# Optimization experiments

Measured on AMD Instinct MI355X. Metric: run time of the kernel, lower is better.

Reference implementation:

```python
import jax, jax.numpy as jnp
import numpy as np

B, S, HID = 2, 2048, 2048
NH, NKV, D = 16, 4, 128
EPS = 1e-6
THETA = 1000000.0
SCALE = D ** -0.5


def _rmsnorm(x, w):
    # per-head RMSNorm over last dim (head_dim)
    var = jnp.mean(x * x, axis=-1, keepdims=True)
    return x * jax.lax.rsqrt(var + EPS) * w


def _rope(pos, x):
    # neox-style rotary over full head_dim. x: [B,S,h,D], pos: [B,S]
    half = D // 2
    inv_freq = THETA ** (-jnp.arange(half, dtype=jnp.float32) / half)  # theta^(-2i/D)
    freqs = pos.astype(jnp.float32)[..., None] * inv_freq              # [B,S,half]
    cos = jnp.cos(freqs)[:, :, None, :]
    sin = jnp.sin(freqs)[:, :, None, :]
    x1, x2 = x[..., :half], x[..., half:]
    return jnp.concatenate([x1 * cos - x2 * sin, x2 * cos + x1 * sin], axis=-1)


def setup_inputs() -> dict:
    key = jax.random.key(0)
    ks = jax.random.split(key, 6)
    hidden_states = jax.random.normal(ks[0], (B, S, HID), dtype=jnp.float32)
    positions = jnp.tile(jnp.arange(S, dtype=jnp.int32)[None, :], (B, 1))
    sd = 0.02
    Wq = jax.random.normal(ks[1], (HID, NH * D), dtype=jnp.float32) * sd
    Wk = jax.random.normal(ks[2], (HID, NKV * D), dtype=jnp.float32) * sd
    Wv = jax.random.normal(ks[3], (HID, NKV * D), dtype=jnp.float32) * sd
    Wo = jax.random.normal(ks[4], (NH * D, HID), dtype=jnp.float32) * sd
    q_norm_w = jnp.ones((D,), dtype=jnp.float32)
    k_norm_w = jnp.ones((D,), dtype=jnp.float32)
    return {"hidden_states": hidden_states, "positions": positions,
            "Wq": Wq, "Wk": Wk, "Wv": Wv, "Wo": Wo,
            "q_norm_w": q_norm_w, "k_norm_w": k_norm_w}


def reference(hidden_states, positions, Wq, Wk, Wv, Wo, q_norm_w, k_norm_w):
    # QKV projections (no bias)
    q = (hidden_states @ Wq).reshape(B, S, NH, D)
    k = (hidden_states @ Wk).reshape(B, S, NKV, D)
    v = (hidden_states @ Wv).reshape(B, S, NKV, D)
    # per-head RMSNorm
    q = _rmsnorm(q, q_norm_w)
    k = _rmsnorm(k, k_norm_w)
    # rotary embedding
    q = _rope(positions, q)
    k = _rope(positions, k)
    # GQA: expand kv heads to q heads
    rep = NH // NKV
    k = jnp.repeat(k, rep, axis=2)  # [B,S,NH,D]
    v = jnp.repeat(v, rep, axis=2)
    # non-causal (ENCODER_ONLY) attention
    scores = jnp.einsum('bqhd,bkhd->bhqk', q, k) * SCALE
    attn = jax.nn.softmax(scores, axis=-1)
    ctx = jnp.einsum('bhqk,bkhd->bqhd', attn, v).reshape(B, S, NH * D)
    out = ctx @ Wo
    return out
```

## Files before the change

kernel.cpp:

```cpp
#include <hip/hip_runtime.h>

typedef unsigned short ushort_t;
typedef __attribute__((ext_vector_type(8))) short short8;
typedef __attribute__((ext_vector_type(4))) float f32x4;

#define Bb 2
#define Ss 2048
#define HID 2048
#define NH 16
#define NKV 4
#define Dd 128
constexpr float EPS_ = 1e-6f;
constexpr float THETA_ = 1000000.0f;
constexpr float SCALE_ = 0.08838834764831845f;
constexpr float C2_ = 0.12753785f;

__device__ __forceinline__ ushort_t f2bf(float x) {
  union { float f; unsigned u; } v; v.f = x;
  unsigned r = (v.u + 0x7fffu + ((v.u >> 16) & 1u)) >> 16;
  return (ushort_t)r;
}
__device__ __forceinline__ float bf2f(ushort_t u) {
  union { unsigned u; float f; } v; v.u = ((unsigned)u) << 16;
  return v.f;
}

typedef const __attribute__((address_space(1))) void* gas1_t;
typedef __attribute__((address_space(3))) void* las3_t;
__device__ __forceinline__ void gload_lds16(const void* g, void* l) {
  __builtin_amdgcn_global_load_lds((gas1_t)g, (las3_t)l, 16, 0, 0);
}

__device__ __forceinline__ void store_out(float* p, float v) { *p = v; }
__device__ __forceinline__ void store_out(ushort_t* p, float v) { *p = f2bf(v); }

__global__ __launch_bounds__(256) void convert_f32_bf16(
    const float* __restrict__ src, ushort_t* __restrict__ dst, long n) {
  long i = ((long)blockIdx.x * 256 + threadIdx.x) * 4;
  if (i + 3 < n) {
    float4 v = *(const float4*)(src + i);
    ushort_t o0 = f2bf(v.x), o1 = f2bf(v.y), o2 = f2bf(v.z), o3 = f2bf(v.w);
    ushort_t* d = dst + i;
    d[0] = o0; d[1] = o1; d[2] = o2; d[3] = o3;
  }
}

__global__ __launch_bounds__(256) void transpose_f32_bf16(
    const float* __restrict__ src, ushort_t* __restrict__ dst, int R, int C) {
  __shared__ float tile[32][33];
  int c0 = blockIdx.x * 32, r0 = blockIdx.y * 32;
  int tx = threadIdx.x & 31, ty = threadIdx.x >> 5;
#pragma unroll
  for (int j = 0; j < 4; j++)
    tile[ty + j * 8][tx] = src[(long)(r0 + ty + j * 8) * C + c0 + tx];
  __syncthreads();
#pragma unroll
  for (int j = 0; j < 4; j++)
    dst[(long)(c0 + ty + j * 8) * R + r0 + tx] = f2bf(tile[tx][ty + j * 8]);
}

template <typename OutT>
__global__ __launch_bounds__(256) void gemm_bt(
    const ushort_t* __restrict__ A, const ushort_t* __restrict__ Bt,
    OutT* __restrict__ C, int M, int N, int K) {
  __shared__ __align__(16) ushort_t As[128 * 32];
  __shared__ __align__(16) ushort_t Bs[128 * 32];
  const int t = threadIdx.x;
  const int wave = t >> 6, lane = t & 63;
  const int wr = wave >> 1, wc = wave & 1;
  const int quad = lane >> 4, l16 = lane & 15;
  const long bm = (long)blockIdx.y * 128, bn = (long)blockIdx.x * 128;

  f32x4 acc[4][4] = {};

  const int srow = t >> 2, schunk = t & 3;
  const ushort_t* aSrc = A + (bm + srow) * (long)K + schunk * 8;
  const ushort_t* bSrc = Bt + (bn + srow) * (long)K + schunk * 8;
  const int ldsOff = srow * 32 + schunk * 8;

  for (int k0 = 0; k0 < K; k0 += 32) {
    __syncthreads();
    gload_lds16(aSrc + k0, &As[ldsOff]);
    gload_lds16(aSrc + (long)64 * K + k0, &As[ldsOff + 64 * 32]);
    gload_lds16(bSrc + k0, &Bs[ldsOff]);
    gload_lds16(bSrc + (long)64 * K + k0, &Bs[ldsOff + 64 * 32]);
    __syncthreads();
    short8 af[4], bf[4];
#pragma unroll
    for (int i = 0; i < 4; i++) {
      af[i] = *(const short8*)&As[(wr * 64 + i * 16 + l16) * 32 + quad * 8];
      bf[i] = *(const short8*)&Bs[(wc * 64 + i * 16 + l16) * 32 + quad * 8];
    }
#pragma unroll
    for (int i = 0; i < 4; i++)
#pragma unroll
      for (int j = 0; j < 4; j++)
        acc[i][j] = __builtin_amdgcn_mfma_f32_16x16x32_bf16(af[i], bf[j], acc[i][j], 0, 0, 0);
  }
#pragma unroll
  for (int i = 0; i < 4; i++)
#pragma unroll
    for (int j = 0; j < 4; j++)
#pragma unroll
      for (int r = 0; r < 4; r++) {
        long rr = bm + wr * 64 + i * 16 + quad * 4 + r;
        long cc = bn + wc * 64 + j * 16 + l16;
        store_out(&C[rr * N + cc], acc[i][j][r]);
      }
}

__global__ __launch_bounds__(256) void rmsnorm_rope(
    ushort_t* __restrict__ qkv, const int* __restrict__ positions,
    const float* __restrict__ qw, const float* __restrict__ kw) {
  int gw = blockIdx.x * 4 + (threadIdx.x >> 6);
  int lane = threadIdx.x & 63;
  int bs = gw / 20, h = gw % 20;
  ushort_t* src = qkv + (long)bs * 3072 + h * 128;
  float x0 = bf2f(src[lane]), x1 = bf2f(src[lane + 64]);
  float ss = x0 * x0 + x1 * x1;
#pragma unroll
  for (int off = 32; off; off >>= 1) ss += __shfl_xor(ss, off);
  float r = rsqrtf(ss * (1.0f / 128.0f) + EPS_);
  const float* w = (h < 16) ? qw : kw;
  x0 = x0 * r * w[lane];
  x1 = x1 * r * w[lane + 64];
  float pos = (float)positions[bs];
  float inv_freq = powf(THETA_, -(float)lane * (1.0f / 64.0f));
  float f = pos * inv_freq;
  float sn, cs;
  sincosf(f, &sn, &cs);
  float o0 = x0 * cs - x1 * sn;
  float o1 = x1 * cs + x0 * sn;
  src[lane] = f2bf(o0);
  src[lane + 64] = f2bf(o1);
}

__global__ __launch_bounds__(256) void transpose_v(
    const ushort_t* __restrict__ qkv, ushort_t* __restrict__ Vt) {
  __shared__ ushort_t tile[64][65];
  int bh = blockIdx.z;
  int s0 = blockIdx.x * 64, d0 = blockIdx.y * 64;
  int b = bh >> 2, hk = bh & 3;
  int tx = threadIdx.x & 63, ty = threadIdx.x >> 6;
#pragma unroll
  for (int j = 0; j < 16; j++) {
    int sl = j * 4 + ty;
    tile[sl][tx] = qkv[(long)(b * Ss + s0 + sl) * 3072 + 2560 + hk * 128 + d0 + tx];
  }
  __syncthreads();
  const long vtbase = (long)bh * Dd * Ss;
#pragma unroll
  for (int j = 0; j < 16; j++) {
    int dl = j * 4 + ty;
    Vt[vtbase + (long)(d0 + dl) * Ss + s0 + tx] = tile[tx][dl];
  }
}

__global__ __launch_bounds__(512) void flash_attn(
    const ushort_t* __restrict__ qkv, const ushort_t* __restrict__ Vt,
    ushort_t* __restrict__ ctx) {
  __shared__ __align__(16) ushort_t Ks[2][64 * 128];
  __shared__ __align__(16) ushort_t Vs[2][128 * 64];
  __shared__ __align__(16) ushort_t Ps[8][16 * 64];
  const int qt = blockIdx.x, h = blockIdx.y, b = blockIdx.z;
  const int hk = h >> 2;
  const int t = threadIdx.x, wave = t >> 6, lane = t & 63;
  const int quad = lane >> 4, l16 = lane & 15;

  const ushort_t* qp = qkv + (long)(b * Ss + qt * 128) * 3072 + h * 128;
  const ushort_t* kp = qkv + (long)(b * Ss) * 3072 + 2048 + hk * 128;
  const ushort_t* vp = Vt + ((long)(b * NKV + hk) * Dd) * Ss;

  auto stage = [&](int kt, int bi) {
    const int k0 = kt * 64;
#pragma unroll
    for (int it = 0; it < 2; it++) {
      int tt = t + it * 512;
      int row = tt >> 4, cl = tt & 15, cg = cl ^ (row & 15);
      gload_lds16(kp + (long)(k0 + row) * 3072 + cg * 8, &Ks[bi][tt * 8]);
    }
#pragma unroll
    for (int it = 0; it < 2; it++) {
      int tt = t + it * 512;
      int row = tt >> 3, cl = tt & 7, cg = cl ^ (row & 7);
      gload_lds16(vp + (long)row * Ss + k0 + cg * 8, &Vs[bi][tt * 8]);
    }
  };

  stage(0, 0);

  short8 qf[4];
  {
    const ushort_t* qrow = qp + (long)(wave * 16 + l16) * 3072 + quad * 8;
#pragma unroll
    for (int kc = 0; kc < 4; kc++)
      qf[kc] = *(const short8*)(qrow + kc * 32);
  }

  float m_i[4] = {-1e30f, -1e30f, -1e30f, -1e30f};
  float l_i[4] = {0.f, 0.f, 0.f, 0.f};
  f32x4 o[8] = {};

  asm volatile("s_waitcnt vmcnt(0)" ::: "memory");
  __syncthreads();

  int cur = 0;
  for (int kt = 0; kt < Ss / 64; kt++) {
    if (kt + 1 < Ss / 64) stage(kt + 1, cur ^ 1);

    f32x4 sa[4] = {};
#pragma unroll
    for (int kc = 0; kc < 4; kc++) {
#pragma unroll
      for (int nt = 0; nt < 4; nt++) {
        int brow = nt * 16 + l16;
        short8 bfr = *(const short8*)&Ks[cur][brow * 128 + (((kc * 4 + quad) ^ (brow & 15)) * 8)];
        sa[nt] = __builtin_amdgcn_mfma_f32_16x16x32_bf16(qf[kc], bfr, sa[nt], 0, 0, 0);
      }
    }

    float mc[4], alpha[4];
#pragma unroll
    for (int r = 0; r < 4; r++) {
      float mx = fmaxf(fmaxf(sa[0][r], sa[1][r]), fmaxf(sa[2][r], sa[3][r]));
#pragma unroll
      for (int off = 8; off; off >>= 1) mx = fmaxf(mx, __shfl_xor(mx, off));
      float mnew = fmaxf(m_i[r], mx);
      alpha[r] = __builtin_amdgcn_exp2f((m_i[r] - mnew) * C2_);
      m_i[r] = mnew;
      mc[r] = mnew * C2_;
    }
    float rs[4] = {0.f, 0.f, 0.f, 0.f};
#pragma unroll
    for (int nt = 0; nt < 4; nt++)
#pragma unroll
      for (int r = 0; r < 4; r++) {
        float p = __builtin_amdgcn_exp2f(__builtin_fmaf(sa[nt][r], C2_, -mc[r]));
        sa[nt][r] = p;
        rs[r] += p;
      }
#pragma unroll
    for (int r = 0; r < 4; r++) {
#pragma unroll
      for (int off = 8; off; off >>= 1) rs[r] += __shfl_xor(rs[r], off);
      l_i[r] = l_i[r] * alpha[r] + rs[r];
    }
#pragma unroll
    for (int nt = 0; nt < 4; nt++)
#pragma unroll
      for (int r = 0; r < 4; r++) {
        int row = quad * 4 + r, col = nt * 16 + l16;
        int cg = col >> 3, ci = col & 7;
        int cl = cg ^ (row & 7);
        union { float f; unsigned u; } pv; pv.f = sa[nt][r];
        Ps[wave][row * 64 + cl * 8 + ci] = (ushort_t)((pv.u + 0x8000u) >> 16);
      }
#pragma unroll
    for (int dt = 0; dt < 8; dt++)
#pragma unroll
      for (int r = 0; r < 4; r++) o[dt][r] *= alpha[r];
    asm volatile("s_waitcnt lgkmcnt(0)" ::: "memory");
#pragma unroll
    for (int kc = 0; kc < 2; kc++) {
      int arow = l16;
      short8 af = *(const short8*)&Ps[wave][arow * 64 + (((kc * 4 + quad) ^ (arow & 7)) * 8)];
#pragma unroll
      for (int dt = 0; dt < 8; dt++) {
        int brow = dt * 16 + l16;
        short8 bfr = *(const short8*)&Vs[cur][brow * 64 + (((kc * 4 + quad) ^ (brow & 7)) * 8)];
        o[dt] = __builtin_amdgcn_mfma_f32_16x16x32_bf16(af, bfr, o[dt], 0, 0, 0);
      }
    }

    asm volatile("s_waitcnt vmcnt(0)" ::: "memory");
    __syncthreads();
    cur ^= 1;
  }
  const long obase = (long)(b * Ss + qt * 128 + wave * 16) * (NH * Dd) + h * Dd;
#pragma unroll
  for (int dt = 0; dt < 8; dt++)
#pragma unroll
    for (int r = 0; r < 4; r++) {
      int row = quad * 4 + r, col = dt * 16 + l16;
      ctx[obase + (long)row * (NH * Dd) + col] = f2bf(o[dt][r] / l_i[r]);
    }
}

extern "C" void kernel_launch(void* const* d_in, const int* in_sizes, int n_in,
                              void* d_out, int out_size, void* d_ws, size_t ws_size,
                              hipStream_t stream) {
  const float* hidden = (const float*)d_in[0];
  const int* positions = (const int*)d_in[1];
  const float* Wq = (const float*)d_in[2];
  const float* Wk = (const float*)d_in[3];
  const float* Wv = (const float*)d_in[4];
  const float* Wo = (const float*)d_in[5];
  const float* qw = (const float*)d_in[6];
  const float* kw = (const float*)d_in[7];
  float* out = (float*)d_out;

  char* ws = (char*)d_ws;
  ushort_t* Xbf = (ushort_t*)(ws);
  ushort_t* WqkvT = (ushort_t*)(ws + (16l << 20));
  ushort_t* WoT = (ushort_t*)(ws + (28l << 20));
  ushort_t* qkvb = (ushort_t*)(ws + (36l << 20));
  ushort_t* Vt = (ushort_t*)(ws + (60l << 20));
  ushort_t* ctx = Xbf;

  const long nX = (long)Bb * Ss * HID;
  convert_f32_bf16<<<(unsigned)(nX / 4 / 256), 256, 0, stream>>>(hidden, Xbf, nX);
  transpose_f32_bf16<<<dim3(2048 / 32, 2048 / 32), 256, 0, stream>>>(Wq, WqkvT, 2048, 2048);
  transpose_f32_bf16<<<dim3(512 / 32, 2048 / 32), 256, 0, stream>>>(Wk, WqkvT + (long)2048 * 2048, 2048, 512);
  transpose_f32_bf16<<<dim3(512 / 32, 2048 / 32), 256, 0, stream>>>(Wv, WqkvT + (long)2560 * 2048, 2048, 512);
  transpose_f32_bf16<<<dim3(2048 / 32, 2048 / 32), 256, 0, stream>>>(Wo, WoT, 2048, 2048);

  gemm_bt<ushort_t><<<dim3(3072 / 128, 4096 / 128), 256, 0, stream>>>(Xbf, WqkvT, qkvb, 4096, 3072, 2048);

  rmsnorm_rope<<<(Bb * Ss * 20) / 4, 256, 0, stream>>>(qkvb, positions, qw, kw);
  transpose_v<<<dim3(Ss / 64, Dd / 64, Bb * NKV), 256, 0, stream>>>(qkvb, Vt);

  flash_attn<<<dim3(Ss / 128, NH, Bb), 512, 0, stream>>>(qkvb, Vt, ctx);

  gemm_bt<float><<<dim3(2048 / 128, 4096 / 128), 256, 0, stream>>>(ctx, WoT, out, 4096, 2048, 2048);
}
```

Before: 406.9 us.

## Use lazy max rescaling, deferred row-sum reduction and MFMA priority in attention

Online softmax now moves the running max, and rescales the output accumulator, only when a new block max exceeds the old one by a raw-score threshold. Otherwise the stale max is kept and the rescale is skipped. The per-row sum is kept per lane and reduced across lanes once after the loop instead of every tile, and the final divide becomes one reciprocal-multiply. s_setprio is raised around the MFMA sections so this wave is favoured while they issue. Exponentials may exceed 1 under the stale max (bounded by the threshold, about 2^3), which adds some bf16 rounding risk for P.

```diff
diff --git a/kernel.cpp b/kernel.cpp
--- a/kernel.cpp
+++ b/kernel.cpp
@@ -14,6 +14,7 @@
 constexpr float THETA_ = 1000000.0f;
 constexpr float SCALE_ = 0.08838834764831845f;
 constexpr float C2_ = 0.12753785f;
+constexpr float THR_RAW_ = 23.5f;
 
 __device__ __forceinline__ ushort_t f2bf(float x) {
   union { float f; unsigned u; } v; v.f = x;
@@ -198,7 +199,7 @@
   }
 
   float m_i[4] = {-1e30f, -1e30f, -1e30f, -1e30f};
-  float l_i[4] = {0.f, 0.f, 0.f, 0.f};
+  float l_acc[4] = {0.f, 0.f, 0.f, 0.f};
   f32x4 o[8] = {};
 
   asm volatile("s_waitcnt vmcnt(0)" ::: "memory");
@@ -209,6 +210,7 @@
     if (kt + 1 < Ss / 64) stage(kt + 1, cur ^ 1);
 
     f32x4 sa[4] = {};
+    __builtin_amdgcn_s_setprio(1);
 #pragma unroll
     for (int kc = 0; kc < 4; kc++) {
 #pragma unroll
@@ -218,17 +220,21 @@
         sa[nt] = __builtin_amdgcn_mfma_f32_16x16x32_bf16(qf[kc], bfr, sa[nt], 0, 0, 0);
       }
     }
+    __builtin_amdgcn_s_setprio(0);
 
     float mc[4], alpha[4];
+    bool upd[4];
 #pragma unroll
     for (int r = 0; r < 4; r++) {
       float mx = fmaxf(fmaxf(sa[0][r], sa[1][r]), fmaxf(sa[2][r], sa[3][r]));
 #pragma unroll
       for (int off = 8; off; off >>= 1) mx = fmaxf(mx, __shfl_xor(mx, off));
-      float mnew = fmaxf(m_i[r], mx);
-      alpha[r] = __builtin_amdgcn_exp2f((m_i[r] - mnew) * C2_);
-      m_i[r] = mnew;
-      mc[r] = mnew * C2_;
+      float g = mx - m_i[r];
+      upd[r] = g > THR_RAW_;
+      float a = __builtin_amdgcn_exp2f((m_i[r] - mx) * C2_);
+      alpha[r] = upd[r] ? a : 1.0f;
+      m_i[r] = upd[r] ? mx : m_i[r];
+      mc[r] = m_i[r] * C2_;
     }
     float rs[4] = {0.f, 0.f, 0.f, 0.f};
 #pragma unroll
@@ -236,30 +242,23 @@
 #pragma unroll
       for (int r = 0; r < 4; r++) {
         float p = __builtin_amdgcn_exp2f(__builtin_fmaf(sa[nt][r], C2_, -mc[r]));
-        sa[nt][r] = p;
         rs[r] += p;
-      }
-#pragma unroll
-    for (int r = 0; r < 4; r++) {
-#pragma unroll
-      for (int off = 8; off; off >>= 1) rs[r] += __shfl_xor(rs[r], off);
-      l_i[r] = l_i[r] * alpha[r] + rs[r];
-    }
-#pragma unroll
-    for (int nt = 0; nt < 4; nt++)
-#pragma unroll
-      for (int r = 0; r < 4; r++) {
         int row = quad * 4 + r, col = nt * 16 + l16;
         int cg = col >> 3, ci = col & 7;
         int cl = cg ^ (row & 7);
-        union { float f; unsigned u; } pv; pv.f = sa[nt][r];
+        union { float f; unsigned u; } pv; pv.f = p;
         Ps[wave][row * 64 + cl * 8 + ci] = (ushort_t)((pv.u + 0x8000u) >> 16);
       }
 #pragma unroll
-    for (int dt = 0; dt < 8; dt++)
-#pragma unroll
-      for (int r = 0; r < 4; r++) o[dt][r] *= alpha[r];
+    for (int r = 0; r < 4; r++) l_acc[r] = l_acc[r] * alpha[r] + rs[r];
+    if (upd[0] | upd[1] | upd[2] | upd[3]) {
+#pragma unroll
+      for (int dt = 0; dt < 8; dt++)
+#pragma unroll
+        for (int r = 0; r < 4; r++) o[dt][r] *= alpha[r];
+    }
     asm volatile("s_waitcnt lgkmcnt(0)" ::: "memory");
+    __builtin_amdgcn_s_setprio(1);
 #pragma unroll
     for (int kc = 0; kc < 2; kc++) {
       int arow = l16;
@@ -271,18 +270,25 @@
         o[dt] = __builtin_amdgcn_mfma_f32_16x16x32_bf16(af, bfr, o[dt], 0, 0, 0);
       }
     }
+    __builtin_amdgcn_s_setprio(0);
 
     asm volatile("s_waitcnt vmcnt(0)" ::: "memory");
     __syncthreads();
     cur ^= 1;
   }
+#pragma unroll
+  for (int r = 0; r < 4; r++) {
+#pragma unroll
+    for (int off = 8; off; off >>= 1) l_acc[r] += __shfl_xor(l_acc[r], off);
+    l_acc[r] = 1.0f / l_acc[r];
+  }
   const long obase = (long)(b * Ss + qt * 128 + wave * 16) * (NH * Dd) + h * Dd;
 #pragma unroll
   for (int dt = 0; dt < 8; dt++)
 #pragma unroll
     for (int r = 0; r < 4; r++) {
       int row = quad * 4 + r, col = dt * 16 + l16;
-      ctx[obase + (long)row * (NH * Dd) + col] = f2bf(o[dt][r] / l_i[r]);
+      ctx[obase + (long)row * (NH * Dd) + col] = f2bf(o[dt][r] * l_acc[r]);
     }
 }
 
```

After: 425.4 us. +4.5%, slower.

## Compute transposed S tile so each lane owns one query row in softmax

Applied to the files above, without the earlier changes.

Swaps the MFMA operands so the score tile comes out transposed, with each lane's registers holding a single query row. The row max and row sum then need only two cross-lane shuffles instead of per-register four-step butterflies, and P is written to LDS in a layout the PV MFMA can read directly. Per-row alpha and 1/l are redistributed with __shfl for rescaling O, and the final division becomes a multiply by the reciprocal. This cuts softmax shuffle and VALU work in the attention inner loop, at the cost of extra broadcast shuffles and a different LDS write pattern for P.

```diff
diff --git a/kernel.cpp b/kernel.cpp
--- a/kernel.cpp
+++ b/kernel.cpp
@@ -197,8 +197,8 @@
       qf[kc] = *(const short8*)(qrow + kc * 32);
   }
 
-  float m_i[4] = {-1e30f, -1e30f, -1e30f, -1e30f};
-  float l_i[4] = {0.f, 0.f, 0.f, 0.f};
+  float m_i = -1e30f;
+  float l_acc = 0.f;
   f32x4 o[8] = {};
 
   asm volatile("s_waitcnt vmcnt(0)" ::: "memory");
@@ -214,52 +214,48 @@
 #pragma unroll
       for (int nt = 0; nt < 4; nt++) {
         int brow = nt * 16 + l16;
-        short8 bfr = *(const short8*)&Ks[cur][brow * 128 + (((kc * 4 + quad) ^ (brow & 15)) * 8)];
-        sa[nt] = __builtin_amdgcn_mfma_f32_16x16x32_bf16(qf[kc], bfr, sa[nt], 0, 0, 0);
+        short8 kfr = *(const short8*)&Ks[cur][brow * 128 + (((kc * 4 + quad) ^ (brow & 15)) * 8)];
+        sa[nt] = __builtin_amdgcn_mfma_f32_16x16x32_bf16(kfr, qf[kc], sa[nt], 0, 0, 0);
       }
     }
 
-    float mc[4], alpha[4];
-#pragma unroll
-    for (int r = 0; r < 4; r++) {
-      float mx = fmaxf(fmaxf(sa[0][r], sa[1][r]), fmaxf(sa[2][r], sa[3][r]));
-#pragma unroll
-      for (int off = 8; off; off >>= 1) mx = fmaxf(mx, __shfl_xor(mx, off));
-      float mnew = fmaxf(m_i[r], mx);
-      alpha[r] = __builtin_amdgcn_exp2f((m_i[r] - mnew) * C2_);
-      m_i[r] = mnew;
-      mc[r] = mnew * C2_;
-    }
-    float rs[4] = {0.f, 0.f, 0.f, 0.f};
+    float pmax = sa[0][0];
 #pragma unroll
     for (int nt = 0; nt < 4; nt++)
 #pragma unroll
+      for (int r = 0; r < 4; r++) pmax = fmaxf(pmax, sa[nt][r]);
+    float mx = fmaxf(pmax, __shfl_xor(pmax, 16));
+    mx = fmaxf(mx, __shfl_xor(mx, 32));
+
+    float mnew = fmaxf(m_i, mx);
+    float alpha = __builtin_amdgcn_exp2f((m_i - mnew) * C2_);
+    m_i = mnew;
+    float mC2 = mnew * C2_;
+
+    float rs = 0.f;
+#pragma unroll
+    for (int nt = 0; nt < 4; nt++) {
+      int cbase = l16 * 64 + ((nt * 2 + (quad >> 1)) ^ (l16 & 7)) * 8 + (quad & 1) * 4;
+#pragma unroll
       for (int r = 0; r < 4; r++) {
-        float p = __builtin_amdgcn_exp2f(__builtin_fmaf(sa[nt][r], C2_, -mc[r]));
-        sa[nt][r] = p;
-        rs[r] += p;
+        float p = __builtin_amdgcn_exp2f(__builtin_fmaf(sa[nt][r], C2_, -mC2));
+        rs += p;
+        union { float f; unsigned u; } pv; pv.f = p;
+        Ps[wave][cbase + r] = (ushort_t)((pv.u + 0x8000u) >> 16);
       }
-#pragma unroll
-    for (int r = 0; r < 4; r++) {
-#pragma unroll
-      for (int off = 8; off; off >>= 1) rs[r] += __shfl_xor(rs[r], off);
-      l_i[r] = l_i[r] * alpha[r] + rs[r];
-    }
-#pragma unroll
-    for (int nt = 0; nt < 4; nt++)
-#pragma unroll
-      for (int r = 0; r < 4; r++) {
-        int row = quad * 4 + r, col = nt * 16 + l16;
-        int cg = col >> 3, ci = col & 7;
-        int cl = cg ^ (row & 7);
-        union { float f; unsigned u; } pv; pv.f = sa[nt][r];
-        Ps[wave][row * 64 + cl * 8 + ci] = (ushort_t)((pv.u + 0x8000u) >> 16);
-      }
-#pragma unroll
-    for (int dt = 0; dt < 8; dt++)
-#pragma unroll
-      for (int r = 0; r < 4; r++) o[dt][r] *= alpha[r];
+    }
+    l_acc = l_acc * alpha + rs;
+
+    float ar0 = __shfl(alpha, quad * 4 + 0);
+    float ar1 = __shfl(alpha, quad * 4 + 1);
+    float ar2 = __shfl(alpha, quad * 4 + 2);
+    float ar3 = __shfl(alpha, quad * 4 + 3);
+#pragma unroll
+    for (int dt = 0; dt < 8; dt++) {
+      o[dt][0] *= ar0; o[dt][1] *= ar1; o[dt][2] *= ar2; o[dt][3] *= ar3;
+    }
     asm volatile("s_waitcnt lgkmcnt(0)" ::: "memory");
+
 #pragma unroll
     for (int kc = 0; kc < 2; kc++) {
       int arow = l16;
@@ -276,14 +272,23 @@
     __syncthreads();
     cur ^= 1;
   }
+
+  float lt = l_acc + __shfl_xor(l_acc, 16);
+  lt += __shfl_xor(lt, 32);
+  float linv = 1.0f / lt;
+  float lr0 = __shfl(linv, quad * 4 + 0);
+  float lr1 = __shfl(linv, quad * 4 + 1);
+  float lr2 = __shfl(linv, quad * 4 + 2);
+  float lr3 = __shfl(linv, quad * 4 + 3);
   const long obase = (long)(b * Ss + qt * 128 + wave * 16) * (NH * Dd) + h * Dd;
 #pragma unroll
-  for (int dt = 0; dt < 8; dt++)
-#pragma unroll
-    for (int r = 0; r < 4; r++) {
-      int row = quad * 4 + r, col = dt * 16 + l16;
-      ctx[obase + (long)row * (NH * Dd) + col] = f2bf(o[dt][r] / l_i[r]);
-    }
+  for (int dt = 0; dt < 8; dt++) {
+    int col = dt * 16 + l16;
+    ctx[obase + (long)(quad * 4 + 0) * (NH * Dd) + col] = f2bf(o[dt][0] * lr0);
+    ctx[obase + (long)(quad * 4 + 1) * (NH * Dd) + col] = f2bf(o[dt][1] * lr1);
+    ctx[obase + (long)(quad * 4 + 2) * (NH * Dd) + col] = f2bf(o[dt][2] * lr2);
+    ctx[obase + (long)(quad * 4 + 3) * (NH * Dd) + col] = f2bf(o[dt][3] * lr3);
+  }
 }
 
 extern "C" void kernel_launch(void* const* d_in, const int* in_sizes, int n_in,
```

Measured after the change: 370.4 us. -9.0%, faster.
